# Performance work log

Hardware: AMD Instinct MI355X
Metric: run time of the kernel (lower is better)

The kernel has to match this reference:

```python
import jax, jax.numpy as jnp
import numpy as np

T, B, D_IN, D_H = 512, 64, 1024, 1024
NOISE_STD = 0.01

def setup_inputs() -> dict:
    key = jax.random.key(0)
    k_x, k_n, k_w, k_b = jax.random.split(key, 4)
    inputs = jax.random.normal(k_x, (T, B, D_IN), dtype=jnp.float32)
    # _init_states: zeros + the SAME gaussian noise added to both hx and cx
    noise = jax.random.normal(k_n, (B, D_H), dtype=jnp.float32) * NOISE_STD
    hx0 = noise
    cx0 = noise
    # nn.Linear(input_dim+hidden_dim, 4*hidden_dim): W [4H, D_in+H], b [4H]
    fan_in = D_IN + D_H
    bound = 1.0 / np.sqrt(fan_in)
    W = jax.random.uniform(k_w, (4 * D_H, fan_in), dtype=jnp.float32, minval=-bound, maxval=bound)
    b = jax.random.uniform(k_b, (4 * D_H,), dtype=jnp.float32, minval=-bound, maxval=bound)
    return {"inputs": inputs, "hx0": hx0, "cx0": cx0, "W": W, "b": b}

def reference(inputs, hx0, cx0, W, b):
    Wt = W.T  # [D_in+H, 4H]

    def step(carry, x_t):
        hx, cx = carry
        combined = jnp.concatenate([x_t, hx], axis=1)          # [B, D_in+H]
        gates = combined @ Wt + b                              # [B, 4H]
        f, i, g, o = jnp.split(gates, 4, axis=1)               # chunk order f,i,g,o
        f = jax.nn.sigmoid(f)
        i = jax.nn.sigmoid(i)
        g = jnp.tanh(g)
        o = jax.nn.sigmoid(o)
        cx = f * cx + i * g
        hx = o * jnp.tanh(cx)
        return (hx, cx), hx

    (hx, cx), stacked = jax.lax.scan(step, (hx0, cx0), inputs)
    return stacked, (hx, cx)
```

## Files before the change

kernel.cpp:

```cpp
#include <hip/hip_runtime.h>

#define T_STEPS 512
#define BH      65536
#define STACK   (T_STEPS * BH)
#define NBLK    256
#define NTHR    256

__device__ __forceinline__ float sigf(float x)  { return 1.0f / (1.0f + __expf(-x)); }
__device__ __forceinline__ float tanhf_(float x){ return 2.0f / (1.0f + __expf(-2.0f * x)) - 1.0f; }

__device__ __forceinline__ void dot4(float& a, const float4& w, const float4& c) {
  a = fmaf(w.x, c.x, a);
  a = fmaf(w.y, c.y, a);
  a = fmaf(w.z, c.z, a);
  a = fmaf(w.w, c.w, a);
}

__device__ __forceinline__ void grid_barrier(int* ws, int phase, int blk, int tid) {
  __syncthreads();
  if (tid == 0) {
    const int g = blk & 7;
    __hip_atomic_fetch_add(&ws[g * 64], 1, __ATOMIC_RELEASE, __HIP_MEMORY_SCOPE_AGENT);
    if (blk < 8) {
      while (__hip_atomic_load(&ws[blk * 64], __ATOMIC_RELAXED, __HIP_MEMORY_SCOPE_AGENT) < 32 * (phase + 1))
        __builtin_amdgcn_s_sleep(1);
      (void)__hip_atomic_load(&ws[blk * 64], __ATOMIC_ACQUIRE, __HIP_MEMORY_SCOPE_AGENT);
      __hip_atomic_fetch_add(&ws[512], 1, __ATOMIC_RELEASE, __HIP_MEMORY_SCOPE_AGENT);
    }
    while (__hip_atomic_load(&ws[512], __ATOMIC_RELAXED, __HIP_MEMORY_SCOPE_AGENT) < 8 * (phase + 1))
      __builtin_amdgcn_s_sleep(1);
    (void)__hip_atomic_load(&ws[512], __ATOMIC_ACQUIRE, __HIP_MEMORY_SCOPE_AGENT);
  }
  __syncthreads();
}

__global__ __launch_bounds__(NTHR, 1)
void lstm_k(const float* __restrict__ X, const float* __restrict__ hx0,
            const float* __restrict__ cx0, const float* __restrict__ W,
            const float* __restrict__ bias, float* __restrict__ out,
            int* __restrict__ ws)
{
  __shared__ float part[4160];

  const int tid  = threadIdx.x;
  const int blk  = blockIdx.x;
  const int sw   = tid >> 6;
  const int lane = tid & 63;
  const int bq   = lane >> 2;
  const int gq   = lane & 3;
  const int bb   = tid >> 2;
  const int jj   = tid & 3;
  const int col  = blk * 4 + jj;

  if (tid == 0) __threadfence_system();
  grid_barrier(ws, 0, blk, tid);

  const float bv0 = bias[col], bv1 = bias[1024 + col],
              bv2 = bias[2048 + col], bv3 = bias[3072 + col];
  float creg = cx0[(size_t)bb * 1024 + col];

  const float4* wp[4];
#pragma unroll
  for (int u = 0; u < 4; ++u)
    wp[u] = reinterpret_cast<const float4*>(
        W + (size_t)(gq * 1024 + blk * 4 + u) * 2048 + sw * 256);

  const float4* xb[4];
#pragma unroll
  for (int bi = 0; bi < 4; ++bi)
    xb[bi] = reinterpret_cast<const float4*>(
        X + (size_t)(bq * 4 + bi) * 1024 + sw * 256);

  float acc[4][4];

  for (int t = 0; t < T_STEPS; ++t) {
#pragma unroll
    for (int u = 0; u < 4; ++u)
#pragma unroll
      for (int bi = 0; bi < 4; ++bi) acc[u][bi] = 0.0f;

    const float4* xt0 = xb[0] + (size_t)t * (BH / 4);
    const float4* xt1 = xb[1] + (size_t)t * (BH / 4);
    const float4* xt2 = xb[2] + (size_t)t * (BH / 4);
    const float4* xt3 = xb[3] + (size_t)t * (BH / 4);
#pragma unroll 4
    for (int g = 0; g < 64; ++g) {
      float4 w0 = wp[0][g], w1 = wp[1][g], w2 = wp[2][g], w3 = wp[3][g];
      float4 c0 = xt0[g], c1 = xt1[g], c2 = xt2[g], c3 = xt3[g];
      dot4(acc[0][0], w0, c0); dot4(acc[0][1], w0, c1); dot4(acc[0][2], w0, c2); dot4(acc[0][3], w0, c3);
      dot4(acc[1][0], w1, c0); dot4(acc[1][1], w1, c1); dot4(acc[1][2], w1, c2); dot4(acc[1][3], w1, c3);
      dot4(acc[2][0], w2, c0); dot4(acc[2][1], w2, c1); dot4(acc[2][2], w2, c2); dot4(acc[2][3], w2, c3);
      dot4(acc[3][0], w3, c0); dot4(acc[3][1], w3, c1); dot4(acc[3][2], w3, c2); dot4(acc[3][3], w3, c3);
    }

    const float* hsrc = (t == 0) ? hx0 : out + (size_t)(t - 1) * BH;
    const float4* h0 = reinterpret_cast<const float4*>(hsrc + (size_t)(bq * 4 + 0) * 1024 + sw * 256);
    const float4* h1 = reinterpret_cast<const float4*>(hsrc + (size_t)(bq * 4 + 1) * 1024 + sw * 256);
    const float4* h2 = reinterpret_cast<const float4*>(hsrc + (size_t)(bq * 4 + 2) * 1024 + sw * 256);
    const float4* h3 = reinterpret_cast<const float4*>(hsrc + (size_t)(bq * 4 + 3) * 1024 + sw * 256);
    const float4* q0 = wp[0] + 256;
    const float4* q1 = wp[1] + 256;
    const float4* q2 = wp[2] + 256;
    const float4* q3 = wp[3] + 256;
#pragma unroll 4
    for (int g = 0; g < 64; ++g) {
      float4 w0 = q0[g], w1 = q1[g], w2 = q2[g], w3 = q3[g];
      float4 c0 = h0[g], c1 = h1[g], c2 = h2[g], c3 = h3[g];
      dot4(acc[0][0], w0, c0); dot4(acc[0][1], w0, c1); dot4(acc[0][2], w0, c2); dot4(acc[0][3], w0, c3);
      dot4(acc[1][0], w1, c0); dot4(acc[1][1], w1, c1); dot4(acc[1][2], w1, c2); dot4(acc[1][3], w1, c3);
      dot4(acc[2][0], w2, c0); dot4(acc[2][1], w2, c1); dot4(acc[2][2], w2, c2); dot4(acc[2][3], w2, c3);
      dot4(acc[3][0], w3, c0); dot4(acc[3][1], w3, c1); dot4(acc[3][2], w3, c2); dot4(acc[3][3], w3, c3);
    }

#pragma unroll
    for (int u = 0; u < 4; ++u)
#pragma unroll
      for (int bi = 0; bi < 4; ++bi)
        part[sw * 1040 + (gq * 4 + u) * 65 + bq * 4 + bi] = acc[u][bi];
    __syncthreads();

    float v0 = bv0, v1 = bv1, v2 = bv2, v3 = bv3;
#pragma unroll
    for (int ss = 0; ss < 4; ++ss) {
      v0 += part[ss * 1040 + jj * 65 + bb];
      v1 += part[ss * 1040 + (4 + jj) * 65 + bb];
      v2 += part[ss * 1040 + (8 + jj) * 65 + bb];
      v3 += part[ss * 1040 + (12 + jj) * 65 + bb];
    }
    const float fg = sigf(v0), ig = sigf(v1), gg = tanhf_(v2), og = sigf(v3);
    creg = fg * creg + ig * gg;
    const float hh = og * tanhf_(creg);

    __hip_atomic_store(out + (size_t)t * BH + (size_t)bb * 1024 + col, hh,
                       __ATOMIC_RELAXED, __HIP_MEMORY_SCOPE_AGENT);

    if (t == T_STEPS - 1) {
      out[(size_t)STACK + (size_t)bb * 1024 + col] = hh;
      out[(size_t)STACK + BH + (size_t)bb * 1024 + col] = creg;
    } else {
      grid_barrier(ws, t + 1, blk, tid);
    }
  }
}

extern "C" void kernel_launch(void* const* d_in, const int* in_sizes, int n_in,
                              void* d_out, int out_size, void* d_ws, size_t ws_size,
                              hipStream_t stream) {
  (void)in_sizes; (void)n_in; (void)out_size; (void)ws_size;
  const float* X    = (const float*)d_in[0];
  const float* hx0  = (const float*)d_in[1];
  const float* cx0  = (const float*)d_in[2];
  const float* W    = (const float*)d_in[3];
  const float* bias = (const float*)d_in[4];
  float* out = (float*)d_out;
  int* ws = (int*)d_ws;

  hipMemsetAsync(d_ws, 0, 4096, stream);
  lstm_k<<<dim3(NBLK), dim3(NTHR), 0, stream>>>(X, hx0, cx0, W, bias, out, ws);
}
```

Baseline: 41.72 ms.

## Split grid barrier to overlap input projection, double threads per block

Splits the grid barrier into separate arrive and wait phases so each block computes the input-projection half of the next step's gate GEMV before waiting for the other blocks' hidden state. It also doubles the threads per block to 512, halving each warp's K-slice and reducing over 8 partial sums in shared memory. Hidden-state stores now use sc0/sc1 global stores and relaxed atomics with an explicit vmcnt wait instead of release/acquire atomics. This cuts the serialized per-step latency, but the memory-ordering scheme is more fragile and higher register pressure may affect the GEMV loop.

```diff
diff --git a/kernel.cpp b/kernel.cpp
--- a/kernel.cpp
+++ b/kernel.cpp
@@ -4,7 +4,7 @@
 #define BH      65536
 #define STACK   (T_STEPS * BH)
 #define NBLK    256
-#define NTHR    256
+#define NTHR    512
 
 __device__ __forceinline__ float sigf(float x)  { return 1.0f / (1.0f + __expf(-x)); }
 __device__ __forceinline__ float tanhf_(float x){ return 2.0f / (1.0f + __expf(-2.0f * x)) - 1.0f; }
@@ -16,31 +16,38 @@
   a = fmaf(w.w, c.w, a);
 }
 
-__device__ __forceinline__ void grid_barrier(int* ws, int phase, int blk, int tid) {
+__device__ __forceinline__ void store_llc(float* p, float v) {
+  asm volatile("global_store_dword %0, %1, off sc0 sc1" :: "v"(p), "v"(v) : "memory");
+}
+
+__device__ __forceinline__ void barrier_arrive(int* ws, int blk, int tid) {
+  asm volatile("s_waitcnt vmcnt(0)" ::: "memory");
   __syncthreads();
+  if (tid == 0)
+    __hip_atomic_fetch_add(&ws[(blk & 7) * 64], 1, __ATOMIC_RELAXED, __HIP_MEMORY_SCOPE_AGENT);
+}
+
+__device__ __forceinline__ void barrier_wait(int* ws, int n, int blk, int tid) {
   if (tid == 0) {
-    const int g = blk & 7;
-    __hip_atomic_fetch_add(&ws[g * 64], 1, __ATOMIC_RELEASE, __HIP_MEMORY_SCOPE_AGENT);
     if (blk < 8) {
-      while (__hip_atomic_load(&ws[blk * 64], __ATOMIC_RELAXED, __HIP_MEMORY_SCOPE_AGENT) < 32 * (phase + 1))
+      while (__hip_atomic_load(&ws[blk * 64], __ATOMIC_RELAXED, __HIP_MEMORY_SCOPE_AGENT) < 32 * n)
         __builtin_amdgcn_s_sleep(1);
-      (void)__hip_atomic_load(&ws[blk * 64], __ATOMIC_ACQUIRE, __HIP_MEMORY_SCOPE_AGENT);
-      __hip_atomic_fetch_add(&ws[512], 1, __ATOMIC_RELEASE, __HIP_MEMORY_SCOPE_AGENT);
+      __hip_atomic_fetch_add(&ws[512], 1, __ATOMIC_RELAXED, __HIP_MEMORY_SCOPE_AGENT);
     }
-    while (__hip_atomic_load(&ws[512], __ATOMIC_RELAXED, __HIP_MEMORY_SCOPE_AGENT) < 8 * (phase + 1))
+    while (__hip_atomic_load(&ws[512], __ATOMIC_RELAXED, __HIP_MEMORY_SCOPE_AGENT) < 8 * n)
       __builtin_amdgcn_s_sleep(1);
-    (void)__hip_atomic_load(&ws[512], __ATOMIC_ACQUIRE, __HIP_MEMORY_SCOPE_AGENT);
   }
   __syncthreads();
+  asm volatile("" ::: "memory");
 }
 
-__global__ __launch_bounds__(NTHR, 1)
+__global__ __launch_bounds__(NTHR, 2)
 void lstm_k(const float* __restrict__ X, const float* __restrict__ hx0,
             const float* __restrict__ cx0, const float* __restrict__ W,
             const float* __restrict__ bias, float* __restrict__ out,
             int* __restrict__ ws)
 {
-  __shared__ float part[4160];
+  __shared__ float part[8 * 1040];
 
   const int tid  = threadIdx.x;
   const int blk  = blockIdx.x;
@@ -52,27 +59,32 @@
   const int jj   = tid & 3;
   const int col  = blk * 4 + jj;
 
-  if (tid == 0) __threadfence_system();
-  grid_barrier(ws, 0, blk, tid);
-
-  const float bv0 = bias[col], bv1 = bias[1024 + col],
-              bv2 = bias[2048 + col], bv3 = bias[3072 + col];
-  float creg = cx0[(size_t)bb * 1024 + col];
-
-  const float4* wp[4];
+  const float4* wx[4];
+  const float4* wh[4];
 #pragma unroll
-  for (int u = 0; u < 4; ++u)
-    wp[u] = reinterpret_cast<const float4*>(
-        W + (size_t)(gq * 1024 + blk * 4 + u) * 2048 + sw * 256);
-
+  for (int u = 0; u < 4; ++u) {
+    wx[u] = reinterpret_cast<const float4*>(
+        W + (size_t)(gq * 1024 + blk * 4 + u) * 2048 + sw * 128);
+    wh[u] = wx[u] + 256;
+  }
   const float4* xb[4];
 #pragma unroll
   for (int bi = 0; bi < 4; ++bi)
     xb[bi] = reinterpret_cast<const float4*>(
-        X + (size_t)(bq * 4 + bi) * 1024 + sw * 256);
+        X + (size_t)(bq * 4 + bi) * 1024 + sw * 128);
+
+  float bv0 = 0.f, bv1 = 0.f, bv2 = 0.f, bv3 = 0.f, creg = 0.f;
+  if (tid < 256) {
+    bv0 = bias[col]; bv1 = bias[1024 + col]; bv2 = bias[2048 + col]; bv3 = bias[3072 + col];
+    creg = cx0[(size_t)bb * 1024 + col];
+  }
+
+  barrier_arrive(ws, blk, tid);
+  barrier_wait(ws, 1, blk, tid);
 
   float acc[4][4];
 
+#pragma unroll 1
   for (int t = 0; t < T_STEPS; ++t) {
 #pragma unroll
     for (int u = 0; u < 4; ++u)
@@ -84,8 +96,8 @@
     const float4* xt2 = xb[2] + (size_t)t * (BH / 4);
     const float4* xt3 = xb[3] + (size_t)t * (BH / 4);
 #pragma unroll 4
-    for (int g = 0; g < 64; ++g) {
-      float4 w0 = wp[0][g], w1 = wp[1][g], w2 = wp[2][g], w3 = wp[3][g];
+    for (int g = 0; g < 32; ++g) {
+      float4 w0 = wx[0][g], w1 = wx[1][g], w2 = wx[2][g], w3 = wx[3][g];
       float4 c0 = xt0[g], c1 = xt1[g], c2 = xt2[g], c3 = xt3[g];
       dot4(acc[0][0], w0, c0); dot4(acc[0][1], w0, c1); dot4(acc[0][2], w0, c2); dot4(acc[0][3], w0, c3);
       dot4(acc[1][0], w1, c0); dot4(acc[1][1], w1, c1); dot4(acc[1][2], w1, c2); dot4(acc[1][3], w1, c3);
@@ -93,18 +105,16 @@
       dot4(acc[3][0], w3, c0); dot4(acc[3][1], w3, c1); dot4(acc[3][2], w3, c2); dot4(acc[3][3], w3, c3);
     }
 
+    if (t > 0) barrier_wait(ws, t + 1, blk, tid);
+
     const float* hsrc = (t == 0) ? hx0 : out + (size_t)(t - 1) * BH;
-    const float4* h0 = reinterpret_cast<const float4*>(hsrc + (size_t)(bq * 4 + 0) * 1024 + sw * 256);
-    const float4* h1 = reinterpret_cast<const float4*>(hsrc + (size_t)(bq * 4 + 1) * 1024 + sw * 256);
-    const float4* h2 = reinterpret_cast<const float4*>(hsrc + (size_t)(bq * 4 + 2) * 1024 + sw * 256);
-    const float4* h3 = reinterpret_cast<const float4*>(hsrc + (size_t)(bq * 4 + 3) * 1024 + sw * 256);
-    const float4* q0 = wp[0] + 256;
-    const float4* q1 = wp[1] + 256;
-    const float4* q2 = wp[2] + 256;
-    const float4* q3 = wp[3] + 256;
+    const float4* h0 = reinterpret_cast<const float4*>(hsrc + (size_t)(bq * 4 + 0) * 1024 + sw * 128);
+    const float4* h1 = reinterpret_cast<const float4*>(hsrc + (size_t)(bq * 4 + 1) * 1024 + sw * 128);
+    const float4* h2 = reinterpret_cast<const float4*>(hsrc + (size_t)(bq * 4 + 2) * 1024 + sw * 128);
+    const float4* h3 = reinterpret_cast<const float4*>(hsrc + (size_t)(bq * 4 + 3) * 1024 + sw * 128);
 #pragma unroll 4
-    for (int g = 0; g < 64; ++g) {
-      float4 w0 = q0[g], w1 = q1[g], w2 = q2[g], w3 = q3[g];
+    for (int g = 0; g < 32; ++g) {
+      float4 w0 = wh[0][g], w1 = wh[1][g], w2 = wh[2][g], w3 = wh[3][g];
       float4 c0 = h0[g], c1 = h1[g], c2 = h2[g], c3 = h3[g];
       dot4(acc[0][0], w0, c0); dot4(acc[0][1], w0, c1); dot4(acc[0][2], w0, c2); dot4(acc[0][3], w0, c3);
       dot4(acc[1][0], w1, c0); dot4(acc[1][1], w1, c1); dot4(acc[1][2], w1, c2); dot4(acc[1][3], w1, c3);
@@ -119,27 +129,28 @@
         part[sw * 1040 + (gq * 4 + u) * 65 + bq * 4 + bi] = acc[u][bi];
     __syncthreads();
 
-    float v0 = bv0, v1 = bv1, v2 = bv2, v3 = bv3;
+    if (tid < 256) {
+      float v0 = bv0, v1 = bv1, v2 = bv2, v3 = bv3;
 #pragma unroll
-    for (int ss = 0; ss < 4; ++ss) {
-      v0 += part[ss * 1040 + jj * 65 + bb];
-      v1 += part[ss * 1040 + (4 + jj) * 65 + bb];
-      v2 += part[ss * 1040 + (8 + jj) * 65 + bb];
-      v3 += part[ss * 1040 + (12 + jj) * 65 + bb];
+      for (int ss = 0; ss < 8; ++ss) {
+        v0 += part[ss * 1040 + jj * 65 + bb];
+        v1 += part[ss * 1040 + (4 + jj) * 65 + bb];
+        v2 += part[ss * 1040 + (8 + jj) * 65 + bb];
+        v3 += part[ss * 1040 + (12 + jj) * 65 + bb];
+      }
+      const float fg = sigf(v0), ig = sigf(v1), gg = tanhf_(v2), og = sigf(v3);
+      creg = fg * creg + ig * gg;
+      const float hh = og * tanhf_(creg);
+
+      store_llc(out + (size_t)t * BH + (size_t)bb * 1024 + col, hh);
+
+      if (t == T_STEPS - 1) {
+        out[(size_t)STACK + (size_t)bb * 1024 + col] = hh;
+        out[(size_t)STACK + BH + (size_t)bb * 1024 + col] = creg;
+      }
     }
-    const float fg = sigf(v0), ig = sigf(v1), gg = tanhf_(v2), og = sigf(v3);
-    creg = fg * creg + ig * gg;
-    const float hh = og * tanhf_(creg);
 
-    __hip_atomic_store(out + (size_t)t * BH + (size_t)bb * 1024 + col, hh,
-                       __ATOMIC_RELAXED, __HIP_MEMORY_SCOPE_AGENT);
-
-    if (t == T_STEPS - 1) {
-      out[(size_t)STACK + (size_t)bb * 1024 + col] = hh;
-      out[(size_t)STACK + BH + (size_t)bb * 1024 + col] = creg;
-    } else {
-      grid_barrier(ws, t + 1, blk, tid);
-    }
+    if (t < T_STEPS - 1) barrier_arrive(ws, blk, tid);
   }
 }
 
```

Result: faster. 39.79 ms (-4.6%).
